# Kernel tuning notes

Measured on AMD Instinct MI355X. Metric: run time of the kernel, lower is better.

Reference implementation:

```python
import jax, jax.numpy as jnp
import numpy as np
import math

B, L, M = 8, 1024, 1024
H, D, DK, DFF = 16, 1024, 64, 4096
EPS = 1e-5


def _ln(x, g, b):
    mu = jnp.mean(x, axis=-1, keepdims=True)
    var = jnp.mean((x - mu) ** 2, axis=-1, keepdims=True)
    return (x - mu) * jax.lax.rsqrt(var + EPS) * g + b


def _mha(x, kv, Wq, bq, Wk, bk, Wv, bv, Wo, bo, masked):
    # x: [B,Lq,D], kv: [B,Lk,D]; per-head weights stacked: Wq [H,D,DK], bq [H,DK]
    Q = jnp.einsum('bld,hdk->bhlk', x, Wq) + bq[None, :, None, :]
    K = jnp.einsum('bld,hdk->bhlk', kv, Wk) + bk[None, :, None, :]
    V = jnp.einsum('bld,hdk->bhlk', kv, Wv) + bv[None, :, None, :]
    scores = jnp.einsum('bhqk,bhmk->bhqm', Q, K) / math.sqrt(DK)
    p = jax.nn.softmax(scores, axis=-1)
    if masked:
        # faithful to source: mask applied AFTER softmax (multiply by tril ones)
        Lq = x.shape[1]
        tril = jnp.tril(jnp.ones((Lq, kv.shape[1]), dtype=p.dtype))
        p = p * tril
    z = jnp.einsum('bhqm,bhmk->bhqk', p, V)  # [B,H,Lq,DK]
    z = jnp.transpose(z, (0, 2, 1, 3)).reshape(x.shape[0], x.shape[1], H * DK)
    return z @ Wo + bo


def _forward(x, enc, Wq1, bq1, Wk1, bk1, Wv1, bv1, Wo1, bo1,
             Wq2, bq2, Wk2, bk2, Wv2, bv2, Wo2, bo2,
             W1, b1, W2, b2, g1, be1, g2, be2, g3, be3):
    z = _mha(x, x, Wq1, bq1, Wk1, bk1, Wv1, bv1, Wo1, bo1, masked=True)
    x = _ln(z + x, g1, be1)
    z = _mha(x, enc, Wq2, bq2, Wk2, bk2, Wv2, bv2, Wo2, bo2, masked=False)
    x = _ln(z + x, g2, be2)
    # Conv1d(k=1) pair == per-token MLP: relu(x @ W1 + b1) @ W2 + b2
    y = jax.nn.relu(x @ W1 + b1) @ W2 + b2
    return _ln(y + x, g3, be3)


def setup_inputs() -> dict:
    key = jax.random.key(0)
    ks = jax.random.split(key, 16)
    s = 0.02
    return {
        'x': jax.random.normal(ks[0], (B, L, D), jnp.float32),
        'enc': jax.random.normal(ks[1], (B, M, D), jnp.float32),
        'Wq1': jax.random.normal(ks[2], (H, D, DK), jnp.float32) * s,
        'bq1': jnp.zeros((H, DK), jnp.float32),
        'Wk1': jax.random.normal(ks[3], (H, D, DK), jnp.float32) * s,
        'bk1': jnp.zeros((H, DK), jnp.float32),
        'Wv1': jax.random.normal(ks[4], (H, D, DK), jnp.float32) * s,
        'bv1': jnp.zeros((H, DK), jnp.float32),
        'Wo1': jax.random.normal(ks[5], (H * DK, D), jnp.float32) * s,
        'bo1': jnp.zeros((D,), jnp.float32),
        'Wq2': jax.random.normal(ks[6], (H, D, DK), jnp.float32) * s,
        'bq2': jnp.zeros((H, DK), jnp.float32),
        'Wk2': jax.random.normal(ks[7], (H, D, DK), jnp.float32) * s,
        'bk2': jnp.zeros((H, DK), jnp.float32),
        'Wv2': jax.random.normal(ks[8], (H, D, DK), jnp.float32) * s,
        'bv2': jnp.zeros((H, DK), jnp.float32),
        'Wo2': jax.random.normal(ks[9], (H * DK, D), jnp.float32) * s,
        'bo2': jnp.zeros((D,), jnp.float32),
        'W1': jax.random.normal(ks[10], (D, DFF), jnp.float32) * s,
        'b1': jnp.zeros((DFF,), jnp.float32),
        'W2': jax.random.normal(ks[11], (DFF, D), jnp.float32) * s,
        'b2': jnp.zeros((D,), jnp.float32),
        'g1': jnp.ones((D,), jnp.float32), 'be1': jnp.zeros((D,), jnp.float32),
        'g2': jnp.ones((D,), jnp.float32), 'be2': jnp.zeros((D,), jnp.float32),
        'g3': jnp.ones((D,), jnp.float32), 'be3': jnp.zeros((D,), jnp.float32),
    }


def reference(x, enc, Wq1, bq1, Wk1, bk1, Wv1, bv1, Wo1, bo1,
              Wq2, bq2, Wk2, bk2, Wv2, bv2, Wo2, bo2,
              W1, b1, W2, b2, g1, be1, g2, be2, g3, be3):
    return _forward(x, enc, Wq1, bq1, Wk1, bk1, Wv1, bv1, Wo1, bo1,
                    Wq2, bq2, Wk2, bk2, Wv2, bv2, Wo2, bo2,
                    W1, b1, W2, b2, g1, be1, g2, be2, g3, be3)
```

## Files before the change

### kernel.cpp

```cpp
#include <hip/hip_runtime.h>
#include <hip/hip_bf16.h>

typedef __bf16 bf16;
typedef __bf16 bf16x8 __attribute__((ext_vector_type(8)));
typedef __bf16 bf16x4v __attribute__((ext_vector_type(4)));
typedef float f32x4 __attribute__((ext_vector_type(4)));

#define DEV static __device__ __forceinline__

DEV void gll16(const void* g, void* l) {
  __builtin_amdgcn_global_load_lds((__attribute__((address_space(1))) void*)g,
                                   (__attribute__((address_space(3))) void*)l,
                                   16, 0, 0);
}

DEV bf16 tobf(float f) { return (bf16)f; }

__global__ void cast_f2b_kernel(const float* __restrict__ in, bf16* __restrict__ out, int n4) {
  int i = blockIdx.x * 256 + threadIdx.x;
  if (i < n4) {
    const float4 v = ((const float4*)in)[i];
    bf16x4v o;
    o[0] = tobf(v.x); o[1] = tobf(v.y); o[2] = tobf(v.z); o[3] = tobf(v.w);
    ((bf16x4v*)out)[i] = o;
  }
}

__global__ __launch_bounds__(256)
void tpack_kernel(const float* __restrict__ in, bf16* __restrict__ out,
                  int K, int N, int in_hs, int out_hs, float scale) {
  __shared__ float tile[32][33];
  const int k0 = blockIdx.x << 5, n0 = blockIdx.y << 5;
  const float* ip = in + (size_t)blockIdx.z * in_hs;
  bf16* op = out + (size_t)blockIdx.z * out_hs;
  const int tx = threadIdx.x & 31, ty = threadIdx.x >> 5;
#pragma unroll
  for (int r = 0; r < 4; ++r)
    tile[ty * 4 + r][tx] = ip[(size_t)(k0 + ty * 4 + r) * N + n0 + tx];
  __syncthreads();
#pragma unroll
  for (int r = 0; r < 4; ++r)
    op[(size_t)(n0 + ty * 4 + r) * K + k0 + tx] = tobf(tile[tx][ty * 4 + r] * scale);
}

__global__ void bscale_kernel(const float* __restrict__ in, float* __restrict__ out, int n, float s) {
  int i = blockIdx.x * 256 + threadIdx.x;
  if (i < n) out[i] = in[i] * s;
}

template<int EPI>
__global__ __launch_bounds__(256, 2)
void gemm_bt(const bf16* __restrict__ A, const bf16* __restrict__ W,
             const float* __restrict__ bias, const float* __restrict__ resid,
             void* __restrict__ outv, int M, int N, int K) {
  __shared__ bf16 sA[2][128 * 64];
  __shared__ bf16 sB[2][128 * 64];
  const int nbx = N >> 7;
  const int nwg = (M >> 7) * nbx;
  int bid = (int)blockIdx.x;
  bid = (bid & 7) * (nwg >> 3) + (bid >> 3);
  const int tm = bid / nbx, tn = bid - tm * nbx;
  const int tid = threadIdx.x;
  const int lane = tid & 63;
  const int w = tid >> 6;
  const int wm = (w >> 1) << 6, wn = (w & 1) << 6;
  const int l15 = lane & 15, l4 = lane >> 4;

  int srow[4], scol[4];
#pragma unroll
  for (int j = 0; j < 4; ++j) {
    int g = tid + (j << 8);
    srow[j] = g >> 3;
    scol[j] = ((g & 7) ^ (srow[j] & 7)) << 3;
  }
  const bf16* Abase = A + (size_t)(tm * 128) * K;
  const bf16* Bbase = W + (size_t)(tn * 128) * K;

  f32x4 acc[4][4] = {};

  const int nt = K >> 6;
  int cur = 0;

  auto stage = [&](int buf, int t) {
    const int kb = t << 6;
#pragma unroll
    for (int j = 0; j < 4; ++j) {
      int g = tid + (j << 8);
      gll16(Abase + (size_t)srow[j] * K + kb + scol[j], &sA[buf][g << 3]);
    }
#pragma unroll
    for (int j = 0; j < 4; ++j) {
      int g = tid + (j << 8);
      gll16(Bbase + (size_t)srow[j] * K + kb + scol[j], &sB[buf][g << 3]);
    }
  };

  stage(0, 0);
  __syncthreads();

  for (int t = 0; t < nt; ++t) {
    if (t + 1 < nt) stage(cur ^ 1, t + 1);
    bf16x8 af[4][2], bfm[4][2];
#pragma unroll
    for (int mi = 0; mi < 4; ++mi)
#pragma unroll
      for (int kk = 0; kk < 2; ++kk) {
        int r = wm + (mi << 4) + l15;
        int off = (r << 7) + (kk << 6) + (l4 << 4);
        off ^= (r & 7) << 4;
        af[mi][kk] = *(const bf16x8*)((const char*)sA[cur] + off);
      }
#pragma unroll
    for (int ni = 0; ni < 4; ++ni)
#pragma unroll
      for (int kk = 0; kk < 2; ++kk) {
        int r = wn + (ni << 4) + l15;
        int off = (r << 7) + (kk << 6) + (l4 << 4);
        off ^= (r & 7) << 4;
        bfm[ni][kk] = *(const bf16x8*)((const char*)sB[cur] + off);
      }
#pragma unroll
    for (int mi = 0; mi < 4; ++mi)
#pragma unroll
      for (int ni = 0; ni < 4; ++ni)
#pragma unroll
        for (int kk = 0; kk < 2; ++kk)
          acc[mi][ni] = __builtin_amdgcn_mfma_f32_16x16x32_bf16(af[mi][kk], bfm[ni][kk],
                                                                acc[mi][ni], 0, 0, 0);
    __syncthreads();
    cur ^= 1;
  }

  const int row0 = tm * 128 + wm + (l4 << 2);
  const int col0 = tn * 128 + wn + l15;
#pragma unroll
  for (int ni = 0; ni < 4; ++ni) {
    const int col = col0 + (ni << 4);
    const float bv = bias ? bias[col] : 0.f;
#pragma unroll
    for (int mi = 0; mi < 4; ++mi) {
      const int rr = row0 + (mi << 4);
      f32x4 v = acc[mi][ni];
      if (EPI == 0) {
        bf16* out = (bf16*)outv;
#pragma unroll
        for (int r = 0; r < 4; ++r) out[(size_t)(rr + r) * N + col] = tobf(v[r] + bv);
      } else if (EPI == 1) {
        float* out = (float*)outv;
#pragma unroll
        for (int r = 0; r < 4; ++r) {
          size_t idx = (size_t)(rr + r) * N + col;
          out[idx] = v[r] + bv + resid[idx];
        }
      } else if (EPI == 2) {
        bf16* out = (bf16*)outv;
#pragma unroll
        for (int r = 0; r < 4; ++r) out[(size_t)(rr + r) * N + col] = tobf(fmaxf(v[r] + bv, 0.f));
      } else {
        bf16* out = (bf16*)outv;
        const int bb = rr >> 10, l0 = rr & 1023;
        const int hh = col >> 6, dk = col & 63;
        bf16x4v pk;
#pragma unroll
        for (int r = 0; r < 4; ++r) pk[r] = tobf(v[r] + bv);
        *(bf16x4v*)(out + ((size_t)((bb * 16 + hh) * 64 + dk) << 10) + l0) = pk;
      }
    }
  }
}

template<bool MASKED>
__global__ __launch_bounds__(256, 2)
void attn_kernel(const bf16* __restrict__ Qp, const bf16* __restrict__ Kp,
                 const bf16* __restrict__ Vt, bf16* __restrict__ Z) {
  __shared__ bf16 sK[64 * 64];
  __shared__ bf16 sV[64 * 64];
  __shared__ bf16 sP[4][32 * 72];
  const int Lk = 1024;
  const int bh = blockIdx.y, b = bh >> 4, h = bh & 15;
  const int q0 = blockIdx.x << 7;
  const int tid = threadIdx.x, lane = tid & 63, w = tid >> 6;
  const int l15 = lane & 15, l4 = lane >> 4;

  const bf16* Qb = Qp + ((size_t)(b * 1024 + q0 + w * 32)) * 1024 + h * 64;
  bf16x8 qf[2][2];
#pragma unroll
  for (int mi = 0; mi < 2; ++mi)
#pragma unroll
    for (int kk = 0; kk < 2; ++kk)
      qf[mi][kk] = *(const bf16x8*)(Qb + (size_t)((mi << 4) + l15) * 1024 + (kk << 5) + (l4 << 3));

  f32x4 o[4][2] = {};
  float Mr[2][4], Lr[2][4];
#pragma unroll
  for (int mi = 0; mi < 2; ++mi)
#pragma unroll
    for (int r = 0; r < 4; ++r) { Mr[mi][r] = -1e30f; Lr[mi][r] = 0.f; }

  const bf16* Kb = Kp + ((size_t)b * Lk) * 1024 + h * 64;
  const bf16* Vb = Vt + ((size_t)(b * 16 + h)) * 64 * Lk;

  for (int t = 0; t < (Lk >> 6); ++t) {
    const int kv0 = t << 6;
    __syncthreads();
#pragma unroll
    for (int j = 0; j < 2; ++j) {
      int g = tid + (j << 8);
      int r = g >> 3;
      int sc = ((g & 7) ^ (r & 7)) << 3;
      gll16(Kb + (size_t)(kv0 + r) * 1024 + sc, &sK[g << 3]);
      gll16(Vb + (size_t)r * Lk + kv0 + sc, &sV[g << 3]);
    }
    __syncthreads();

    bf16x8 kf[4][2];
#pragma unroll
    for (int n = 0; n < 4; ++n)
#pragma unroll
      for (int kk = 0; kk < 2; ++kk) {
        int r = (n << 4) + l15;
        int off = (r << 7) + (kk << 6) + (l4 << 4);
        off ^= (r & 7) << 4;
        kf[n][kk] = *(const bf16x8*)((const char*)sK + off);
      }
    f32x4 s[4][2] = {};
#pragma unroll
    for (int n = 0; n < 4; ++n)
#pragma unroll
      for (int mi = 0; mi < 2; ++mi)
#pragma unroll
        for (int kk = 0; kk < 2; ++kk)
          s[n][mi] = __builtin_amdgcn_mfma_f32_16x16x32_bf16(qf[mi][kk], kf[n][kk],
                                                             s[n][mi], 0, 0, 0);

#pragma unroll
    for (int mi = 0; mi < 2; ++mi)
#pragma unroll
      for (int r = 0; r < 4; ++r) {
        float tmx = fmaxf(fmaxf(s[0][mi][r], s[1][mi][r]), fmaxf(s[2][mi][r], s[3][mi][r]));
#pragma unroll
        for (int d = 1; d < 16; d <<= 1) tmx = fmaxf(tmx, __shfl_xor(tmx, d, 64));
        const float Mn = fmaxf(Mr[mi][r], tmx);
        const float al = __expf(Mr[mi][r] - Mn);
        float rs = 0.f;
#pragma unroll
        for (int n = 0; n < 4; ++n) {
          float p = __expf(s[n][mi][r] - Mn);
          s[n][mi][r] = p;
          rs += p;
        }
#pragma unroll
        for (int d = 1; d < 16; d <<= 1) rs += __shfl_xor(rs, d, 64);
        Lr[mi][r] = Lr[mi][r] * al + rs;
        Mr[mi][r] = Mn;
#pragma unroll
        for (int nd = 0; nd < 4; ++nd) o[nd][mi][r] *= al;
      }

#pragma unroll
    for (int n = 0; n < 4; ++n)
#pragma unroll
      for (int mi = 0; mi < 2; ++mi)
#pragma unroll
        for (int r = 0; r < 4; ++r) {
          float v = s[n][mi][r];
          if (MASKED) {
            int cg = kv0 + (n << 4) + l15;
            int rg = q0 + (w << 5) + (mi << 4) + (l4 << 2) + r;
            if (cg > rg) v = 0.f;
          }
          sP[w][((mi << 4) + (l4 << 2) + r) * 72 + (n << 4) + l15] = tobf(v);
        }
    __syncthreads();

    bf16x8 vf[4][2], pa[2][2];
#pragma unroll
    for (int nd = 0; nd < 4; ++nd)
#pragma unroll
      for (int kk = 0; kk < 2; ++kk) {
        int r = (nd << 4) + l15;
        int off = (r << 7) + (kk << 6) + (l4 << 4);
        off ^= (r & 7) << 4;
        vf[nd][kk] = *(const bf16x8*)((const char*)sV + off);
      }
#pragma unroll
    for (int mi = 0; mi < 2; ++mi)
#pragma unroll
      for (int kk = 0; kk < 2; ++kk)
        pa[mi][kk] = *(const bf16x8*)((const char*)sP[w] +
                                      ((mi << 4) + l15) * 144 + (kk << 6) + (l4 << 4));
#pragma unroll
    for (int nd = 0; nd < 4; ++nd)
#pragma unroll
      for (int mi = 0; mi < 2; ++mi)
#pragma unroll
        for (int kk = 0; kk < 2; ++kk)
          o[nd][mi] = __builtin_amdgcn_mfma_f32_16x16x32_bf16(pa[mi][kk], vf[nd][kk],
                                                              o[nd][mi], 0, 0, 0);
  }

  float inv[2][4];
#pragma unroll
  for (int mi = 0; mi < 2; ++mi)
#pragma unroll
    for (int r = 0; r < 4; ++r) inv[mi][r] = 1.f / Lr[mi][r];
  bf16* Zb = Z + ((size_t)(b * 1024 + q0 + w * 32)) * 1024 + h * 64;
#pragma unroll
  for (int nd = 0; nd < 4; ++nd)
#pragma unroll
    for (int mi = 0; mi < 2; ++mi)
#pragma unroll
      for (int r = 0; r < 4; ++r)
        Zb[(size_t)((mi << 4) + (l4 << 2) + r) * 1024 + (nd << 4) + l15] =
            tobf(o[nd][mi][r] * inv[mi][r]);
}

__global__ __launch_bounds__(256)
void ln_kernel(const float* __restrict__ in, const float* __restrict__ gw,
               const float* __restrict__ bw, float* __restrict__ outf,
               bf16* __restrict__ outb) {
  const int row = blockIdx.x, tid = threadIdx.x;
  const size_t base = (size_t)row << 10;
  const float4 v = *(const float4*)(in + base + tid * 4);
  float s = v.x + v.y + v.z + v.w;
  float ss = v.x * v.x + v.y * v.y + v.z * v.z + v.w * v.w;
#pragma unroll
  for (int d = 1; d < 64; d <<= 1) { s += __shfl_xor(s, d, 64); ss += __shfl_xor(ss, d, 64); }
  __shared__ float red[8];
  const int w = tid >> 6;
  if ((tid & 63) == 0) { red[w] = s; red[4 + w] = ss; }
  __syncthreads();
  s = red[0] + red[1] + red[2] + red[3];
  ss = red[4] + red[5] + red[6] + red[7];
  const float mu = s * (1.f / 1024.f);
  const float var = ss * (1.f / 1024.f) - mu * mu;
  const float rstd = rsqrtf(var + 1e-5f);
  const float4 g4 = *(const float4*)(gw + tid * 4);
  const float4 b4 = *(const float4*)(bw + tid * 4);
  const float o0 = (v.x - mu) * rstd * g4.x + b4.x;
  const float o1 = (v.y - mu) * rstd * g4.y + b4.y;
  const float o2 = (v.z - mu) * rstd * g4.z + b4.z;
  const float o3 = (v.w - mu) * rstd * g4.w + b4.w;
  if (outf) { float4 of; of.x = o0; of.y = o1; of.z = o2; of.w = o3;
              *(float4*)(outf + base + tid * 4) = of; }
  if (outb) { bf16x4v ob; ob[0] = tobf(o0); ob[1] = tobf(o1); ob[2] = tobf(o2); ob[3] = tobf(o3);
              *(bf16x4v*)(outb + base + tid * 4) = ob; }
}

extern "C" void kernel_launch(void* const* d_in, const int* in_sizes, int n_in,
                              void* d_out, int out_size, void* d_ws, size_t ws_size,
                              hipStream_t stream) {
  const float* x   = (const float*)d_in[0];
  const float* enc = (const float*)d_in[1];
  const float* Wq1 = (const float*)d_in[2];
  const float* bq1 = (const float*)d_in[3];
  const float* Wk1 = (const float*)d_in[4];
  const float* bk1 = (const float*)d_in[5];
  const float* Wv1 = (const float*)d_in[6];
  const float* bv1 = (const float*)d_in[7];
  const float* Wo1 = (const float*)d_in[8];
  const float* bo1 = (const float*)d_in[9];
  const float* Wq2 = (const float*)d_in[10];
  const float* bq2 = (const float*)d_in[11];
  const float* Wk2 = (const float*)d_in[12];
  const float* bk2 = (const float*)d_in[13];
  const float* Wv2 = (const float*)d_in[14];
  const float* bv2 = (const float*)d_in[15];
  const float* Wo2 = (const float*)d_in[16];
  const float* bo2 = (const float*)d_in[17];
  const float* W1  = (const float*)d_in[18];
  const float* b1  = (const float*)d_in[19];
  const float* W2  = (const float*)d_in[20];
  const float* b2  = (const float*)d_in[21];
  const float* g1  = (const float*)d_in[22];
  const float* be1 = (const float*)d_in[23];
  const float* g2  = (const float*)d_in[24];
  const float* be2 = (const float*)d_in[25];
  const float* g3  = (const float*)d_in[26];
  const float* be3 = (const float*)d_in[27];

  char* ws = (char*)d_ws;
  size_t off = 0;
  auto alloc = [&](size_t bytes) { char* p = ws + off; off += (bytes + 255) & ~(size_t)255; return p; };
  const size_t ACT = (size_t)8 * 1024 * 1024 * 2;
  const size_t WSQ = (size_t)1024 * 1024 * 2;

  bf16* xb    = (bf16*)alloc(ACT);
  bf16* encb  = (bf16*)alloc(ACT);
  bf16* Wq1t  = (bf16*)alloc(WSQ);
  bf16* Wk1t  = (bf16*)alloc(WSQ);
  bf16* Wv1t  = (bf16*)alloc(WSQ);
  bf16* Wq2t  = (bf16*)alloc(WSQ);
  bf16* Wk2t  = (bf16*)alloc(WSQ);
  bf16* Wv2t  = (bf16*)alloc(WSQ);
  bf16* Wo1t  = (bf16*)alloc(WSQ);
  bf16* Wo2t  = (bf16*)alloc(WSQ);
  bf16* W1t   = (bf16*)alloc((size_t)4096 * 1024 * 2);
  bf16* W2t   = (bf16*)alloc((size_t)4096 * 1024 * 2);
  float* sbq1 = (float*)alloc(4096);
  float* sbq2 = (float*)alloc(4096);
  char*  S    = alloc((size_t)64 * 1024 * 1024);
  float* rbuf = (float*)alloc((size_t)8 * 1024 * 1024 * 4);
  float* xnf  = (float*)alloc((size_t)8 * 1024 * 1024 * 4);
  bf16*  xnb  = (bf16*)alloc(ACT);

  bf16* q1   = (bf16*)(S);
  bf16* k1   = (bf16*)(S + ACT);
  bf16* vt1  = (bf16*)(S + 2 * ACT);
  bf16* z1   = (bf16*)(S + 3 * ACT);
  bf16* hbuf = (bf16*)S;

  dim3 b256(256);
  cast_f2b_kernel<<<8192, b256, 0, stream>>>(x, xb, 2097152);
  cast_f2b_kernel<<<8192, b256, 0, stream>>>(enc, encb, 2097152);
  tpack_kernel<<<dim3(32, 2, 16), b256, 0, stream>>>(Wq1, Wq1t, 1024, 64, 65536, 65536, 0.125f);
  tpack_kernel<<<dim3(32, 2, 16), b256, 0, stream>>>(Wk1, Wk1t, 1024, 64, 65536, 65536, 1.f);
  tpack_kernel<<<dim3(32, 2, 16), b256, 0, stream>>>(Wv1, Wv1t, 1024, 64, 65536, 65536, 1.f);
  tpack_kernel<<<dim3(32, 2, 16), b256, 0, stream>>>(Wq2, Wq2t, 1024, 64, 65536, 65536, 0.125f);
  tpack_kernel<<<dim3(32, 2, 16), b256, 0, stream>>>(Wk2, Wk2t, 1024, 64, 65536, 65536, 1.f);
  tpack_kernel<<<dim3(32, 2, 16), b256, 0, stream>>>(Wv2, Wv2t, 1024, 64, 65536, 65536, 1.f);
  tpack_kernel<<<dim3(32, 32, 1), b256, 0, stream>>>(Wo1, Wo1t, 1024, 1024, 0, 0, 1.f);
  tpack_kernel<<<dim3(32, 32, 1), b256, 0, stream>>>(Wo2, Wo2t, 1024, 1024, 0, 0, 1.f);
  tpack_kernel<<<dim3(32, 128, 1), b256, 0, stream>>>(W1, W1t, 1024, 4096, 0, 0, 1.f);
  tpack_kernel<<<dim3(128, 32, 1), b256, 0, stream>>>(W2, W2t, 4096, 1024, 0, 0, 1.f);
  bscale_kernel<<<4, b256, 0, stream>>>(bq1, sbq1, 1024, 0.125f);
  bscale_kernel<<<4, b256, 0, stream>>>(bq2, sbq2, 1024, 0.125f);

  gemm_bt<0><<<512, b256, 0, stream>>>(xb, Wq1t, sbq1, nullptr, q1, 8192, 1024, 1024);
  gemm_bt<0><<<512, b256, 0, stream>>>(xb, Wk1t, bk1, nullptr, k1, 8192, 1024, 1024);
  gemm_bt<3><<<512, b256, 0, stream>>>(xb, Wv1t, bv1, nullptr, vt1, 8192, 1024, 1024);
  attn_kernel<true><<<dim3(8, 128), b256, 0, stream>>>(q1, k1, vt1, z1);
  gemm_bt<1><<<512, b256, 0, stream>>>(z1, Wo1t, bo1, x, rbuf, 8192, 1024, 1024);
  ln_kernel<<<8192, b256, 0, stream>>>(rbuf, g1, be1, xnf, xnb);

  gemm_bt<0><<<512, b256, 0, stream>>>(xnb, Wq2t, sbq2, nullptr, q1, 8192, 1024, 1024);
  gemm_bt<0><<<512, b256, 0, stream>>>(encb, Wk2t, bk2, nullptr, k1, 8192, 1024, 1024);
  gemm_bt<3><<<512, b256, 0, stream>>>(encb, Wv2t, bv2, nullptr, vt1, 8192, 1024, 1024);
  attn_kernel<false><<<dim3(8, 128), b256, 0, stream>>>(q1, k1, vt1, z1);
  gemm_bt<1><<<512, b256, 0, stream>>>(z1, Wo2t, bo2, xnf, rbuf, 8192, 1024, 1024);
  ln_kernel<<<8192, b256, 0, stream>>>(rbuf, g2, be2, xnf, xnb);

  gemm_bt<2><<<2048, b256, 0, stream>>>(xnb, W1t, b1, nullptr, hbuf, 8192, 4096, 1024);
  gemm_bt<1><<<512, b256, 0, stream>>>(hbuf, W2t, b2, xnf, rbuf, 8192, 1024, 4096);
  ln_kernel<<<8192, b256, 0, stream>>>(rbuf, g3, be3, (float*)d_out, nullptr);
}
```

Measured before the change: 686.6 us.

## Double-buffer attention K/V tiles and skip masked-out PV work

The attention kernel now double-buffers K and V tiles in shared memory, prefetching the next tile while computing the current one, so each step needs one barrier instead of two. In the masked (post-softmax tril) case, the P·V product and the V loads are skipped for KV tiles lying entirely above the diagonal, since those probabilities are zeroed anyway. The softmax statistics are still computed over all keys, which keeps the reference's mask-after-softmax semantics. The grid is flattened to 1D with batch-head as the fast index, and the occupancy hint rises to 3 blocks per CU, at the cost of twice the K/V shared memory.

```diff
diff --git a/kernel.cpp b/kernel.cpp
--- a/kernel.cpp
+++ b/kernel.cpp
@@ -77,7 +77,6 @@
   const bf16* Bbase = W + (size_t)(tn * 128) * K;
 
   f32x4 acc[4][4] = {};
-
   const int nt = K >> 6;
   int cur = 0;
 
@@ -170,15 +169,17 @@
 }
 
 template<bool MASKED>
-__global__ __launch_bounds__(256, 2)
+__global__ __launch_bounds__(256, 3)
 void attn_kernel(const bf16* __restrict__ Qp, const bf16* __restrict__ Kp,
                  const bf16* __restrict__ Vt, bf16* __restrict__ Z) {
-  __shared__ bf16 sK[64 * 64];
-  __shared__ bf16 sV[64 * 64];
+  __shared__ bf16 sK[2][64 * 64];
+  __shared__ bf16 sV[2][64 * 64];
   __shared__ bf16 sP[4][32 * 72];
   const int Lk = 1024;
-  const int bh = blockIdx.y, b = bh >> 4, h = bh & 15;
-  const int q0 = blockIdx.x << 7;
+  const int d = blockIdx.x;
+  const int bh = d & 127, qb = d >> 7;
+  const int b = bh >> 4, h = bh & 15;
+  const int q0 = qb << 7;
   const int tid = threadIdx.x, lane = tid & 63, w = tid >> 6;
   const int l15 = lane & 15, l4 = lane >> 4;
 
@@ -200,18 +201,27 @@
   const bf16* Kb = Kp + ((size_t)b * Lk) * 1024 + h * 64;
   const bf16* Vb = Vt + ((size_t)(b * 16 + h)) * 64 * Lk;
 
-  for (int t = 0; t < (Lk >> 6); ++t) {
+  auto stage = [&](int buf, int t, bool withV) {
     const int kv0 = t << 6;
-    __syncthreads();
 #pragma unroll
     for (int j = 0; j < 2; ++j) {
       int g = tid + (j << 8);
       int r = g >> 3;
       int sc = ((g & 7) ^ (r & 7)) << 3;
-      gll16(Kb + (size_t)(kv0 + r) * 1024 + sc, &sK[g << 3]);
-      gll16(Vb + (size_t)r * Lk + kv0 + sc, &sV[g << 3]);
+      gll16(Kb + (size_t)(kv0 + r) * 1024 + sc, &sK[buf][g << 3]);
+      if (withV) gll16(Vb + (size_t)r * Lk + kv0 + sc, &sV[buf][g << 3]);
     }
-    __syncthreads();
+  };
+  auto needPV = [&](int t) -> bool { return !MASKED || ((t << 6) < q0 + 128); };
+
+  const int NT = Lk >> 6;
+  stage(0, 0, true);
+  __syncthreads();
+  int cur = 0;
+
+  for (int t = 0; t < NT; ++t) {
+    if (t + 1 < NT) stage(cur ^ 1, t + 1, needPV(t + 1));
+    const int kv0 = t << 6;
 
     bf16x8 kf[4][2];
 #pragma unroll
@@ -221,7 +231,7 @@
         int r = (n << 4) + l15;
         int off = (r << 7) + (kk << 6) + (l4 << 4);
         off ^= (r & 7) << 4;
-        kf[n][kk] = *(const bf16x8*)((const char*)sK + off);
+        kf[n][kk] = *(const bf16x8*)((const char*)sK[cur] + off);
       }
     f32x4 s[4][2] = {};
 #pragma unroll
@@ -239,7 +249,7 @@
       for (int r = 0; r < 4; ++r) {
         float tmx = fmaxf(fmaxf(s[0][mi][r], s[1][mi][r]), fmaxf(s[2][mi][r], s[3][mi][r]));
 #pragma unroll
-        for (int d = 1; d < 16; d <<= 1) tmx = fmaxf(tmx, __shfl_xor(tmx, d, 64));
+        for (int dd = 1; dd < 16; dd <<= 1) tmx = fmaxf(tmx, __shfl_xor(tmx, dd, 64));
         const float Mn = fmaxf(Mr[mi][r], tmx);
         const float al = __expf(Mr[mi][r] - Mn);
         float rs = 0.f;
@@ -250,53 +260,56 @@
           rs += p;
         }
 #pragma unroll
-        for (int d = 1; d < 16; d <<= 1) rs += __shfl_xor(rs, d, 64);
+        for (int dd = 1; dd < 16; dd <<= 1) rs += __shfl_xor(rs, dd, 64);
         Lr[mi][r] = Lr[mi][r] * al + rs;
         Mr[mi][r] = Mn;
 #pragma unroll
         for (int nd = 0; nd < 4; ++nd) o[nd][mi][r] *= al;
       }
 
-#pragma unroll
-    for (int n = 0; n < 4; ++n)
+    if (needPV(t)) {
+#pragma unroll
+      for (int n = 0; n < 4; ++n)
+#pragma unroll
+        for (int mi = 0; mi < 2; ++mi)
+#pragma unroll
+          for (int r = 0; r < 4; ++r) {
+            float v = s[n][mi][r];
+            if (MASKED) {
+              int cg = kv0 + (n << 4) + l15;
+              int rg = q0 + (w << 5) + (mi << 4) + (l4 << 2) + r;
+              if (cg > rg) v = 0.f;
+            }
+            sP[w][((mi << 4) + (l4 << 2) + r) * 72 + (n << 4) + l15] = tobf(v);
+          }
+
+      bf16x8 vf[4][2], pa[2][2];
+#pragma unroll
+      for (int nd = 0; nd < 4; ++nd)
+#pragma unroll
+        for (int kk = 0; kk < 2; ++kk) {
+          int r = (nd << 4) + l15;
+          int off = (r << 7) + (kk << 6) + (l4 << 4);
+          off ^= (r & 7) << 4;
+          vf[nd][kk] = *(const bf16x8*)((const char*)sV[cur] + off);
+        }
 #pragma unroll
       for (int mi = 0; mi < 2; ++mi)
 #pragma unroll
-        for (int r = 0; r < 4; ++r) {
-          float v = s[n][mi][r];
-          if (MASKED) {
-            int cg = kv0 + (n << 4) + l15;
-            int rg = q0 + (w << 5) + (mi << 4) + (l4 << 2) + r;
-            if (cg > rg) v = 0.f;
-          }
-          sP[w][((mi << 4) + (l4 << 2) + r) * 72 + (n << 4) + l15] = tobf(v);
-        }
+        for (int kk = 0; kk < 2; ++kk)
+          pa[mi][kk] = *(const bf16x8*)((const char*)sP[w] +
+                                        ((mi << 4) + l15) * 144 + (kk << 6) + (l4 << 4));
+#pragma unroll
+      for (int nd = 0; nd < 4; ++nd)
+#pragma unroll
+        for (int mi = 0; mi < 2; ++mi)
+#pragma unroll
+          for (int kk = 0; kk < 2; ++kk)
+            o[nd][mi] = __builtin_amdgcn_mfma_f32_16x16x32_bf16(pa[mi][kk], vf[nd][kk],
+                                                                o[nd][mi], 0, 0, 0);
+    }
     __syncthreads();
-
-    bf16x8 vf[4][2], pa[2][2];
-#pragma unroll
-    for (int nd = 0; nd < 4; ++nd)
-#pragma unroll
-      for (int kk = 0; kk < 2; ++kk) {
-        int r = (nd << 4) + l15;
-        int off = (r << 7) + (kk << 6) + (l4 << 4);
-        off ^= (r & 7) << 4;
-        vf[nd][kk] = *(const bf16x8*)((const char*)sV + off);
-      }
-#pragma unroll
-    for (int mi = 0; mi < 2; ++mi)
-#pragma unroll
-      for (int kk = 0; kk < 2; ++kk)
-        pa[mi][kk] = *(const bf16x8*)((const char*)sP[w] +
-                                      ((mi << 4) + l15) * 144 + (kk << 6) + (l4 << 4));
-#pragma unroll
-    for (int nd = 0; nd < 4; ++nd)
-#pragma unroll
-      for (int mi = 0; mi < 2; ++mi)
-#pragma unroll
-        for (int kk = 0; kk < 2; ++kk)
-          o[nd][mi] = __builtin_amdgcn_mfma_f32_16x16x32_bf16(pa[mi][kk], vf[nd][kk],
-                                                              o[nd][mi], 0, 0, 0);
+    cur ^= 1;
   }
 
   float inv[2][4];
@@ -429,14 +442,14 @@
   gemm_bt<0><<<512, b256, 0, stream>>>(xb, Wq1t, sbq1, nullptr, q1, 8192, 1024, 1024);
   gemm_bt<0><<<512, b256, 0, stream>>>(xb, Wk1t, bk1, nullptr, k1, 8192, 1024, 1024);
   gemm_bt<3><<<512, b256, 0, stream>>>(xb, Wv1t, bv1, nullptr, vt1, 8192, 1024, 1024);
-  attn_kernel<true><<<dim3(8, 128), b256, 0, stream>>>(q1, k1, vt1, z1);
+  attn_kernel<true><<<1024, b256, 0, stream>>>(q1, k1, vt1, z1);
   gemm_bt<1><<<512, b256, 0, stream>>>(z1, Wo1t, bo1, x, rbuf, 8192, 1024, 1024);
   ln_kernel<<<8192, b256, 0, stream>>>(rbuf, g1, be1, xnf, xnb);
 
   gemm_bt<0><<<512, b256, 0, stream>>>(xnb, Wq2t, sbq2, nullptr, q1, 8192, 1024, 1024);
   gemm_bt<0><<<512, b256, 0, stream>>>(encb, Wk2t, bk2, nullptr, k1, 8192, 1024, 1024);
   gemm_bt<3><<<512, b256, 0, stream>>>(encb, Wv2t, bv2, nullptr, vt1, 8192, 1024, 1024);
-  attn_kernel<false><<<dim3(8, 128), b256, 0, stream>>>(q1, k1, vt1, z1);
+  attn_kernel<false><<<1024, b256, 0, stream>>>(q1, k1, vt1, z1);
   gemm_bt<1><<<512, b256, 0, stream>>>(z1, Wo2t, bo2, xnf, rbuf, 8192, 1024, 1024);
   ln_kernel<<<8192, b256, 0, stream>>>(rbuf, g2, be2, xnf, xnb);
 
```

After: 664.0 us. -3.3%, faster.
